# Kernel tuning notes

Measured on AMD Instinct MI355X. Metric: run time of the kernel, lower is better.

## Reference

```python
import jax, jax.numpy as jnp
import numpy as np

M, N, IN, H, NC = 2048, 64, 16, 256, 64
OUT = 3 * NC
NUM_LAYERS = 2


def _lstm_layer(x, Wih, Whh, bih, bhh):
    # x: (M, T, F); Wih: (4H, F); Whh: (4H, H). Torch gate order: i, f, g, o.
    xg = jnp.einsum('mtf,gf->mtg', x, Wih) + bih + bhh  # (M, T, 4H)
    h0 = jnp.zeros((x.shape[0], Whh.shape[1]), x.dtype)

    def step(carry, xt):
        h, c = carry
        gates = xt + h @ Whh.T
        i, f, g, o = jnp.split(gates, 4, axis=-1)
        c = jax.nn.sigmoid(f) * c + jax.nn.sigmoid(i) * jnp.tanh(g)
        h = jax.nn.sigmoid(o) * jnp.tanh(c)
        return (h, c), h

    (_, _), hs = jax.lax.scan(step, (h0, h0), jnp.swapaxes(xg, 0, 1))
    return jnp.swapaxes(hs, 0, 1)  # (M, T, H)


def setup_inputs() -> dict:
    key = jax.random.key(0)
    ks = jax.random.split(key, 12)
    s = 1.0 / np.sqrt(H)
    d = {
        'z': jax.random.normal(ks[0], (M, N, IN), jnp.float32),
        'Wih0': jax.random.normal(ks[1], (4 * H, IN), jnp.float32) * s,
        'Whh0': jax.random.normal(ks[2], (4 * H, H), jnp.float32) * s,
        'bih0': jax.random.normal(ks[3], (4 * H,), jnp.float32) * s,
        'bhh0': jax.random.normal(ks[4], (4 * H,), jnp.float32) * s,
        'Wih1': jax.random.normal(ks[5], (4 * H, H), jnp.float32) * s,
        'Whh1': jax.random.normal(ks[6], (4 * H, H), jnp.float32) * s,
        'bih1': jax.random.normal(ks[7], (4 * H,), jnp.float32) * s,
        'bhh1': jax.random.normal(ks[8], (4 * H,), jnp.float32) * s,
        'fcW': jax.random.normal(ks[9], (OUT, H), jnp.float32) * 0.02,
        'fcb': jax.random.normal(ks[10], (OUT,), jnp.float32) * 0.02,
    }
    return d


def reference(z, Wih0, Whh0, bih0, bhh0, Wih1, Whh1, bih1, bhh1, fcW, fcb):
    h = _lstm_layer(z, Wih0, Whh0, bih0, bhh0)
    h = _lstm_layer(h, Wih1, Whh1, bih1, bhh1)
    y = jnp.einsum('mth,oh->mto', h, fcW) + fcb  # (M, N, 3*NC)

    gammas = jax.nn.softmax(y[..., :NC], axis=2)
    sigmas = jnp.exp(y[..., NC:2 * NC])
    mus = y[..., 2 * NC:]

    key = jax.random.key(42)
    k1, k2 = jax.random.split(key)
    idx = jax.random.categorical(k1, jnp.log(gammas), axis=-1)  # (M, N)
    chosen_mu = jnp.take_along_axis(mus, idx[..., None], axis=2)     # (M, N, 1)
    chosen_sig = jnp.take_along_axis(sigmas, idx[..., None], axis=2)
    eps = jax.random.normal(k2, chosen_mu.shape, jnp.float32)
    x_pred = jax.lax.stop_gradient(chosen_mu + chosen_sig * eps)  # Normal.sample (no grad)

    kern_exp = (x_pred - mus) ** 2                         # broadcast repeat over NC
    kernels = jnp.exp(-0.5 * kern_exp) / sigmas ** 2
    kernels = kernels / ((2.0 * jnp.pi) ** (N / 2) * sigmas ** N)
    x_cond_prob = jnp.einsum('mtc,mtc->mt', gammas, kernels)  # (M, N)
    return x_pred, x_cond_prob
```

## Files before the change

kernel.cpp:

```cpp
#include <hip/hip_runtime.h>
#include <stdint.h>
#include <stddef.h>

#define Mdim 2048
#define Tdim 64
#define INdim 16
#define Hdim 256
#define NCdim 64
#define NUG 64
#define HSLAB (256 * 2048)
#define RSLOTS 16

typedef __attribute__((ext_vector_type(8))) short s16x8;
typedef __attribute__((ext_vector_type(4))) float f32x4;

#define PANEL_US (3 * 16 * 8 * 512)
#define SPOFF 65536
#define BFRAG_US (3 * 8 * 3 * 512)

#define OFF_BFRAG 0
#define OFF_WZ    1179648
#define OFF_BB    (OFF_WZ + 64 * 256)
#define OFF_WFCP  (OFF_BB + 64 * 32)
#define OFF_H0P   (OFF_WFCP + 256 * 64 * 4)
#define OFF_C0    (OFF_H0P + 1572864)
#define OFF_C1    (OFF_C0 + HSLAB)
#define OFF_RINGF (OFF_C1 + HSLAB)
#define OFF_RING2 (OFF_RINGF + 12582912)
#define WS_TOT    (OFF_RING2 + RSLOTS * HSLAB)

#define ROTL32(v, s) (((v) << (s)) | ((v) >> (32 - (s))))

__host__ __device__ inline void tf2x32(uint32_t k0, uint32_t k1, uint32_t x0, uint32_t x1,
                                       uint32_t* o0, uint32_t* o1) {
  uint32_t ks2 = k0 ^ k1 ^ 0x1BD11BDAu;
  x0 += k0; x1 += k1;
  x0 += x1; x1 = ROTL32(x1, 13); x1 ^= x0;
  x0 += x1; x1 = ROTL32(x1, 15); x1 ^= x0;
  x0 += x1; x1 = ROTL32(x1, 26); x1 ^= x0;
  x0 += x1; x1 = ROTL32(x1, 6);  x1 ^= x0;
  x0 += k1; x1 += ks2 + 1u;
  x0 += x1; x1 = ROTL32(x1, 17); x1 ^= x0;
  x0 += x1; x1 = ROTL32(x1, 29); x1 ^= x0;
  x0 += x1; x1 = ROTL32(x1, 16); x1 ^= x0;
  x0 += x1; x1 = ROTL32(x1, 24); x1 ^= x0;
  x0 += ks2; x1 += k0 + 2u;
  x0 += x1; x1 = ROTL32(x1, 13); x1 ^= x0;
  x0 += x1; x1 = ROTL32(x1, 15); x1 ^= x0;
  x0 += x1; x1 = ROTL32(x1, 26); x1 ^= x0;
  x0 += x1; x1 = ROTL32(x1, 6);  x1 ^= x0;
  x0 += k0; x1 += k1 + 3u;
  x0 += x1; x1 = ROTL32(x1, 17); x1 ^= x0;
  x0 += x1; x1 = ROTL32(x1, 29); x1 ^= x0;
  x0 += x1; x1 = ROTL32(x1, 16); x1 ^= x0;
  x0 += x1; x1 = ROTL32(x1, 24); x1 ^= x0;
  x0 += k1; x1 += ks2 + 4u;
  x0 += x1; x1 = ROTL32(x1, 13); x1 ^= x0;
  x0 += x1; x1 = ROTL32(x1, 15); x1 ^= x0;
  x0 += x1; x1 = ROTL32(x1, 26); x1 ^= x0;
  x0 += x1; x1 = ROTL32(x1, 6);  x1 ^= x0;
  x0 += ks2; x1 += k0 + 5u;
  *o0 = x0; *o1 = x1;
}

__device__ inline uint32_t random_bits32(uint32_t ka, uint32_t kb, uint32_t p) {
  uint32_t a, b;
  tf2x32(ka, kb, 0u, p, &a, &b);
  return a ^ b;
}

__device__ inline float bits_to_u01(uint32_t bits) {
  return __uint_as_float((bits >> 9) | 0x3f800000u) - 1.0f;
}

__device__ inline float sigm_fast(float x) { return 1.0f / (1.0f + __expf(-x)); }

__device__ inline float erfinv_f32(float x) {
  float w = -log1pf(-x * x);
  float p;
  if (w < 5.0f) {
    w -= 2.5f;
    p = 2.81022636e-08f;
    p = fmaf(p, w, 3.43273939e-07f);
    p = fmaf(p, w, -3.5233877e-06f);
    p = fmaf(p, w, -4.39150654e-06f);
    p = fmaf(p, w, 0.00021858087f);
    p = fmaf(p, w, -0.00125372503f);
    p = fmaf(p, w, -0.00417768164f);
    p = fmaf(p, w, 0.246640727f);
    p = fmaf(p, w, 1.50140941f);
  } else {
    w = sqrtf(w) - 3.0f;
    p = -0.000200214257f;
    p = fmaf(p, w, 0.000100950558f);
    p = fmaf(p, w, 0.00134934322f);
    p = fmaf(p, w, -0.00367342844f);
    p = fmaf(p, w, 0.00573950773f);
    p = fmaf(p, w, -0.0076224613f);
    p = fmaf(p, w, 0.00943887047f);
    p = fmaf(p, w, 1.00167406f);
    p = fmaf(p, w, 2.83297682f);
  }
  return p * x;
}

__device__ inline void mdn_head(float yg, float ysg, float ym, int lane, uint32_t rid,
                                uint32_t k1a, uint32_t k1b, uint32_t k2a, uint32_t k2b,
                                float* __restrict__ out) {
  uint32_t pp = rid * (uint32_t)NCdim + (uint32_t)lane;
  uint32_t bits = random_bits32(k1a, k1b, pp);
  float u01 = bits_to_u01(bits);
  const float tinyf = 1.17549435e-38f;
  float uu = fmaxf(tinyf, u01 + tinyf);
  float gum = -logf(-logf(uu));
  float val = gum + yg;
  int idx = lane;
#pragma unroll
  for (int s = 1; s < 64; s <<= 1) {
    float ov = __shfl_xor(val, s);
    int oi = __shfl_xor(idx, s);
    if (ov > val || (ov == val && oi < idx)) { val = ov; idx = oi; }
  }
  float mu_sel = __shfl(ym, idx);
  float s_sel = __shfl(ysg, idx);

  uint32_t ebits = random_bits32(k2a, k2b, rid);
  float ue = bits_to_u01(ebits);
  const float lo = __uint_as_float(0xBF7FFFFFu);
  float un2 = fmaxf(lo, ue * 2.0f + lo);
  float eps = 1.41421356f * erfinv_f32(un2);

  float x_pred = mu_sel + expf(s_sel) * eps;

  float mx = yg;
#pragma unroll
  for (int s = 1; s < 64; s <<= 1) mx = fmaxf(mx, __shfl_xor(mx, s));
  float se = expf(yg - mx);
#pragma unroll
  for (int s = 1; s < 64; s <<= 1) se += __shfl_xor(se, s);
  float d = x_pred - ym;
  float lk = -0.5f * d * d - 66.0f * ysg - 58.812066f;
  float ts = expf(yg - mx + lk);
#pragma unroll
  for (int s = 1; s < 64; s <<= 1) ts += __shfl_xor(ts, s);
  float prob = ts / se;

  if (lane == 0) {
    out[rid] = x_pred;
    out[(size_t)Mdim * Tdim + rid] = prob;
  }
}

__device__ __host__ inline unsigned short bf16_trunc(float x) {
  union { float f; uint32_t u; } c; c.f = x;
  return (unsigned short)(c.u >> 16);
}
__device__ __host__ inline float bf16_tof(unsigned short s) {
  union { float f; uint32_t u; } c; c.u = ((uint32_t)s) << 16;
  return c.f;
}

__global__ void vfpg_prep(const float* __restrict__ Wih0, const float* __restrict__ Whh0,
                          const float* __restrict__ Wih1, const float* __restrict__ Whh1,
                          const float* __restrict__ fcW, const float* __restrict__ bih0,
                          const float* __restrict__ bhh0, const float* __restrict__ bih1,
                          const float* __restrict__ bhh1, float* __restrict__ ws) {
  int i0 = blockIdx.x * blockDim.x + threadIdx.x;
  int n = blockDim.x * gridDim.x;
  unsigned short* BF = (unsigned short*)(ws + OFF_BFRAG);
  for (int i = i0; i < 64 * 3 * 8 * 512; i += n) {
    int ug = i / 12288, r = i % 12288;
    int cls = r / 4096, r2 = r % 4096;
    int kt = r2 >> 9, pos = r2 & 511;
    int l = pos >> 3, e = pos & 7;
    int n16 = l & 15, lg = l >> 4;
    int k = kt * 32 + lg * 8 + e;
    int ul = n16 >> 2, ty = n16 & 3;
    int gd = ty * 256 + ug * 4 + ul;
    const float* W = (cls == 0) ? Whh0 : ((cls == 1) ? Wih1 : Whh1);
    float w = W[gd * 256 + k];
    unsigned short s0 = bf16_trunc(w);
    float r1 = w - bf16_tof(s0);
    unsigned short s1 = bf16_trunc(r1);
    unsigned short s2 = bf16_trunc(r1 - bf16_tof(s1));
    size_t base = ((size_t)(ug * 3 + cls) * 8 + kt) * (3 * 512) + pos;
    BF[base] = s0;
    BF[base + 512] = s1;
    BF[base + 1024] = s2;
  }
  for (int i = i0; i < 64 * 256; i += n) {
    int ug = i >> 8, k = (i >> 4) & 15, g = i & 15;
    int gd = (g & 3) * 256 + ug * 4 + (g >> 2);
    ws[OFF_WZ + i] = Wih0[gd * INdim + k];
  }
  for (int i = i0; i < 64 * 32; i += n) {
    int ug = i >> 5, r = i & 31, g = r & 15;
    int gd = (g & 3) * 256 + ug * 4 + (g >> 2);
    ws[OFF_BB + i] = (r < 16) ? (bih0[gd] + bhh0[gd]) : (bih1[gd] + bhh1[gd]);
  }
  float4* wfcp = (float4*)(ws + OFF_WFCP);
  for (int o = i0; o < 256 * 64; o += n) {
    int k = o >> 6, c = o & 63;
    wfcp[o] = make_float4(fcW[c * Hdim + k], fcW[(64 + c) * Hdim + k],
                          fcW[(128 + c) * Hdim + k], 0.0f);
  }
}

__device__ inline void cell1s(float gi, float gf, float gg, float go, float cold,
                              float* cn, float* hn) {
  float si = sigm_fast(gi), sf = sigm_fast(gf);
  float tg = fmaf(2.0f, sigm_fast(2.0f * gg), -1.0f);
  float so = sigm_fast(go);
  float cc = fmaf(sf, cold, si * tg);
  *cn = cc;
  *hn = so * fmaf(2.0f, sigm_fast(2.0f * cc), -1.0f);
}

#define GBS2 33

template <int MODE>
__launch_bounds__(512, 2)
__global__ void vfpg_step(const float* __restrict__ z, const float* __restrict__ ws,
                          float* __restrict__ wsm, int t) {
  __shared__ unsigned short lB01[2 * 2 * 8 * 2 * 512];
  __shared__ __align__(16) unsigned char uni[81920];
  __shared__ float lz[2 * 256];
  __shared__ float lbias[64];

  const int tid = threadIdx.x;
  const int rg = blockIdx.x & 7, ugc = blockIdx.x >> 3;
  const int mb = rg * 256;
  const int lane = tid & 63, wid = tid >> 6;
  float* gbuf = (float*)uni;

  {
    const unsigned short* BF = (const unsigned short*)(ws + OFF_BFRAG);
    const unsigned short* BG0 = BF + (size_t)(ugc * 2 + 0) * BFRAG_US;
    const unsigned short* BG1 = BF + (size_t)(ugc * 2 + 1) * BFRAG_US;
    for (int i = tid; i < 2 * 4608; i += 512) {
      int ugl = i / 4608;
      int r = i % 4608;
      int cls = r / 1536;
      int r2 = r % 1536;
      int kt = r2 / 192;
      int sp = (r2 / 64) % 3;
      int v = r2 & 63;
      const unsigned short* src = (ugl ? BG1 : BG0) + ((size_t)(cls * 8 + kt) * 3 + sp) * 512 + v * 8;
      s16x8 val = *(const s16x8*)src;
      if (cls < 2 && sp < 2) {
        ((s16x8*)lB01)[((((ugl * 2 + cls) * 8 + kt) * 2 + sp)) * 64 + v] = val;
      } else {
        int str = (cls == 2) ? (2 + sp) : cls;
        ((s16x8*)uni)[(((ugl * 5 + str) * 8 + kt)) * 64 + v] = val;
      }
    }
    if (tid < 128) ((float4*)lz)[tid] = ((const float4*)(ws + OFF_WZ + (ugc * 2) * 256))[tid];
    if (tid < 64) lbias[tid] = ws[OFF_BB + (ugc * 2) * 32 + tid];
  }
  __syncthreads();

  f32x4 aL0[2][2], aL1[2][2];
#pragma unroll
  for (int i = 0; i < 2; i++)
#pragma unroll
    for (int u = 0; u < 2; u++) { aL0[i][u] = (f32x4)0.0f; aL1[i][u] = (f32x4)0.0f; }

  if (MODE >= 1) {
    const unsigned short* p0 = (const unsigned short*)(ws + OFF_H0P) +
                               ((size_t)((t - 1) & 1) * 8 + rg) * PANEL_US;
    const unsigned short* p1 = (const unsigned short*)(ws + OFF_RINGF) +
                               ((size_t)((t - 2) & 15) * 8 + rg) * PANEL_US;
    const bool doH1 = (t >= 2);
    const s16x8* pL = (const s16x8*)lB01;
    const s16x8* pU = (const s16x8*)uni;

    s16x8 Ab0[6], Ab1[6];
    {
      size_t fb = ((size_t)(wid * 2) * 8 + 0) * 512 + lane * 8;
      Ab0[0] = *(const s16x8*)(p0 + fb);
      Ab0[1] = *(const s16x8*)(p0 + fb + SPOFF);
      Ab0[2] = *(const s16x8*)(p0 + fb + 2 * SPOFF);
      if (doH1) {
        Ab0[3] = *(const s16x8*)(p1 + fb);
        Ab0[4] = *(const s16x8*)(p1 + fb + SPOFF);
        Ab0[5] = *(const s16x8*)(p1 + fb + 2 * SPOFF);
      }
    }

#pragma unroll 1
    for (int kt = 0; kt < 8; kt++) {
      s16x8 bL0s0[2], bL0s1[2], bL0s2[2], bIs0[2], bIs1[2], bIs2[2], bHs0[2], bHs1[2], bHs2[2];
#pragma unroll
      for (int u = 0; u < 2; u++) {
        if (MODE == 1) {
          bL0s0[u] = pL[(((u * 2 + 0) * 8 + kt) * 2 + 0) * 64 + lane];
          bL0s1[u] = pL[(((u * 2 + 0) * 8 + kt) * 2 + 1) * 64 + lane];
          bL0s2[u] = pU[((u * 5 + 0) * 8 + kt) * 64 + lane];
        }
        bIs0[u] = pL[(((u * 2 + 1) * 8 + kt) * 2 + 0) * 64 + lane];
        bIs1[u] = pL[(((u * 2 + 1) * 8 + kt) * 2 + 1) * 64 + lane];
        bIs2[u] = pU[((u * 5 + 1) * 8 + kt) * 64 + lane];
        if (doH1) {
          bHs0[u] = pU[((u * 5 + 2) * 8 + kt) * 64 + lane];
          bHs1[u] = pU[((u * 5 + 3) * 8 + kt) * 64 + lane];
          bHs2[u] = pU[((u * 5 + 4) * 8 + kt) * 64 + lane];
        }
      }
#pragma unroll
      for (int i = 0; i < 2; i++) {
        s16x8* cur = (i & 1) ? Ab1 : Ab0;
        s16x8* nxt = (i & 1) ? Ab0 : Ab1;
        int nkt = (i < 1) ? kt : kt + 1;
        int ni = (i < 1) ? 1 : 0;
        if (nkt < 8) {
          size_t fb = ((size_t)(wid * 2 + ni) * 8 + nkt) * 512 + lane * 8;
          nxt[0] = *(const s16x8*)(p0 + fb);
          nxt[1] = *(const s16x8*)(p0 + fb + SPOFF);
          nxt[2] = *(const s16x8*)(p0 + fb + 2 * SPOFF);
          if (doH1) {
            nxt[3] = *(const s16x8*)(p1 + fb);
            nxt[4] = *(const s16x8*)(p1 + fb + SPOFF);
            nxt[5] = *(const s16x8*)(p1 + fb + 2 * SPOFF);
          }
        }
        s16x8 a0 = cur[0], a1 = cur[1], a2 = cur[2];
#pragma unroll
        for (int u = 0; u < 2; u++) {
          if (MODE == 1) {
            aL0[i][u] = __builtin_amdgcn_mfma_f32_16x16x32_bf16(a0, bL0s0[u], aL0[i][u], 0, 0, 0);
            aL0[i][u] = __builtin_amdgcn_mfma_f32_16x16x32_bf16(a0, bL0s1[u], aL0[i][u], 0, 0, 0);
            aL0[i][u] = __builtin_amdgcn_mfma_f32_16x16x32_bf16(a1, bL0s0[u], aL0[i][u], 0, 0, 0);
            aL0[i][u] = __builtin_amdgcn_mfma_f32_16x16x32_bf16(a1, bL0s1[u], aL0[i][u], 0, 0, 0);
            aL0[i][u] = __builtin_amdgcn_mfma_f32_16x16x32_bf16(a0, bL0s2[u], aL0[i][u], 0, 0, 0);
            aL0[i][u] = __builtin_amdgcn_mfma_f32_16x16x32_bf16(a2, bL0s0[u], aL0[i][u], 0, 0, 0);
          }
          aL1[i][u] = __builtin_amdgcn_mfma_f32_16x16x32_bf16(a0, bIs0[u], aL1[i][u], 0, 0, 0);
          aL1[i][u] = __builtin_amdgcn_mfma_f32_16x16x32_bf16(a0, bIs1[u], aL1[i][u], 0, 0, 0);
          aL1[i][u] = __builtin_amdgcn_mfma_f32_16x16x32_bf16(a1, bIs0[u], aL1[i][u], 0, 0, 0);
          aL1[i][u] = __builtin_amdgcn_mfma_f32_16x16x32_bf16(a1, bIs1[u], aL1[i][u], 0, 0, 0);
          aL1[i][u] = __builtin_amdgcn_mfma_f32_16x16x32_bf16(a0, bIs2[u], aL1[i][u], 0, 0, 0);
          aL1[i][u] = __builtin_amdgcn_mfma_f32_16x16x32_bf16(a2, bIs0[u], aL1[i][u], 0, 0, 0);
          if (doH1) {
            s16x8 c0 = cur[3], c1 = cur[4], c2 = cur[5];
            aL1[i][u] = __builtin_amdgcn_mfma_f32_16x16x32_bf16(c0, bHs0[u], aL1[i][u], 0, 0, 0);
            aL1[i][u] = __builtin_amdgcn_mfma_f32_16x16x32_bf16(c0, bHs1[u], aL1[i][u], 0, 0, 0);
            aL1[i][u] = __builtin_amdgcn_mfma_f32_16x16x32_bf16(c1, bHs0[u], aL1[i][u], 0, 0, 0);
            aL1[i][u] = __builtin_amdgcn_mfma_f32_16x16x32_bf16(c1, bHs1[u], aL1[i][u], 0, 0, 0);
            aL1[i][u] = __builtin_amdgcn_mfma_f32_16x16x32_bf16(c0, bHs2[u], aL1[i][u], 0, 0, 0);
            aL1[i][u] = __builtin_amdgcn_mfma_f32_16x16x32_bf16(c2, bHs0[u], aL1[i][u], 0, 0, 0);
          }
        }
      }
    }
  }
  __syncthreads();

  float* c0w = wsm + OFF_C0;
  float* c1w = wsm + OFF_C1;
  const int ugl = tid >> 8;
  const int mloc = tid & 255;
  const int m = mb + mloc;
  const int ug = ugc * 2 + ugl;
  const int mtc = mloc >> 4, mrowc = mloc & 15;
  const int ktw = ug >> 3;
  const int lgw = (ug & 7) >> 1;
  const int ebase = (ug * 4) & 7;
  const int lww = lgw * 16 + mrowc;
  const size_t fo = ((size_t)mtc * 8 + ktw) * 512 + lww * 8 + ebase;

  if (MODE <= 1) {
    if (MODE == 1) {
      int col = lane & 15, rb2 = (lane >> 4) * 4;
#pragma unroll
      for (int i = 0; i < 2; i++)
#pragma unroll
        for (int u = 0; u < 2; u++)
#pragma unroll
          for (int j = 0; j < 4; j++)
            gbuf[((wid * 2 + i) * 16 + rb2 + j) * GBS2 + u * 16 + col] = aL0[i][u][j];
    }
    __syncthreads();
    float zr[16];
#pragma unroll
    for (int f4 = 0; f4 < 4; f4++)
      *(float4*)&zr[f4 * 4] = *(const float4*)&z[(size_t)m * 1024 + t * 16 + f4 * 4];
    float g16[16];
#pragma unroll
    for (int gg = 0; gg < 16; gg++)
      g16[gg] = lbias[ugl * 32 + gg] + ((MODE == 1) ? gbuf[mloc * GBS2 + ugl * 16 + gg] : 0.0f);
    const float* lzu = lz + ugl * 256;
#pragma unroll
    for (int f = 0; f < 16; f++) {
      float zv = zr[f];
      float4 w0 = *(const float4*)&lzu[f * 16 + 0];
      float4 w1 = *(const float4*)&lzu[f * 16 + 4];
      float4 w2 = *(const float4*)&lzu[f * 16 + 8];
      float4 w3 = *(const float4*)&lzu[f * 16 + 12];
      g16[0] = fmaf(zv, w0.x, g16[0]);  g16[1] = fmaf(zv, w0.y, g16[1]);
      g16[2] = fmaf(zv, w0.z, g16[2]);  g16[3] = fmaf(zv, w0.w, g16[3]);
      g16[4] = fmaf(zv, w1.x, g16[4]);  g16[5] = fmaf(zv, w1.y, g16[5]);
      g16[6] = fmaf(zv, w1.z, g16[6]);  g16[7] = fmaf(zv, w1.w, g16[7]);
      g16[8] = fmaf(zv, w2.x, g16[8]);  g16[9] = fmaf(zv, w2.y, g16[9]);
      g16[10] = fmaf(zv, w2.z, g16[10]); g16[11] = fmaf(zv, w2.w, g16[11]);
      g16[12] = fmaf(zv, w3.x, g16[12]); g16[13] = fmaf(zv, w3.y, g16[13]);
      g16[14] = fmaf(zv, w3.z, g16[14]); g16[15] = fmaf(zv, w3.w, g16[15]);
    }
    unsigned short* wp = (unsigned short*)(wsm + OFF_H0P) +
                         ((size_t)(t & 1) * 8 + rg) * PANEL_US;
    short sp0[4], sp1[4], sp2[4];
#pragma unroll
    for (int ul = 0; ul < 4; ul++) {
      int u = ug * 4 + ul;
      size_t cidx = (size_t)u * 2048 + m;
      float cold = (MODE == 1) ? c0w[cidx] : 0.0f;
      float cn, hn;
      cell1s(g16[ul * 4 + 0], g16[ul * 4 + 1], g16[ul * 4 + 2], g16[ul * 4 + 3], cold, &cn, &hn);
      c0w[cidx] = cn;
      unsigned short s0 = bf16_trunc(hn);
      float r1 = hn - bf16_tof(s0);
      unsigned short s1 = bf16_trunc(r1);
      unsigned short s2 = bf16_trunc(r1 - bf16_tof(s1));
      sp0[ul] = (short)s0; sp1[ul] = (short)s1; sp2[ul] = (short)s2;
    }
    *(short4*)&wp[fo]             = make_short4(sp0[0], sp0[1], sp0[2], sp0[3]);
    *(short4*)&wp[fo + SPOFF]     = make_short4(sp1[0], sp1[1], sp1[2], sp1[3]);
    *(short4*)&wp[fo + 2 * SPOFF] = make_short4(sp2[0], sp2[1], sp2[2], sp2[3]);
    __syncthreads();
  }

  if (MODE >= 1) {
    {
      int col = lane & 15, rb2 = (lane >> 4) * 4;
#pragma unroll
      for (int i = 0; i < 2; i++)
#pragma unroll
        for (int u = 0; u < 2; u++)
#pragma unroll
          for (int j = 0; j < 4; j++)
            gbuf[((wid * 2 + i) * 16 + rb2 + j) * GBS2 + u * 16 + col] = aL1[i][u][j];
    }
    __syncthreads();
    int slot = (t - 1) & 15;
    unsigned short* rp = (unsigned short*)(wsm + OFF_RINGF) +
                         ((size_t)slot * 8 + rg) * PANEL_US;
    float* r2 = wsm + OFF_RING2 + (size_t)slot * HSLAB;
    float h4[4];
    short sp0[4], sp1[4], sp2[4];
#pragma unroll
    for (int ul = 0; ul < 4; ul++) {
      float gi = lbias[ugl * 32 + 16 + ul * 4 + 0] + gbuf[mloc * GBS2 + ugl * 16 + ul * 4 + 0];
      float gf = lbias[ugl * 32 + 16 + ul * 4 + 1] + gbuf[mloc * GBS2 + ugl * 16 + ul * 4 + 1];
      float gt = lbias[ugl * 32 + 16 + ul * 4 + 2] + gbuf[mloc * GBS2 + ugl * 16 + ul * 4 + 2];
      float go = lbias[ugl * 32 + 16 + ul * 4 + 3] + gbuf[mloc * GBS2 + ugl * 16 + ul * 4 + 3];
      int u = ug * 4 + ul;
      size_t cidx = (size_t)u * 2048 + m;
      float cold = (t >= 2) ? c1w[cidx] : 0.0f;
      float cn, hn;
      cell1s(gi, gf, gt, go, cold, &cn, &hn);
      c1w[cidx] = cn;
      h4[ul] = hn;
      unsigned short s0 = bf16_trunc(hn);
      float r1v = hn - bf16_tof(s0);
      unsigned short s1 = bf16_trunc(r1v);
      unsigned short s2 = bf16_trunc(r1v - bf16_tof(s1));
      sp0[ul] = (short)s0; sp1[ul] = (short)s1; sp2[ul] = (short)s2;
    }
    *(short4*)&rp[fo]             = make_short4(sp0[0], sp0[1], sp0[2], sp0[3]);
    *(short4*)&rp[fo + SPOFF]     = make_short4(sp1[0], sp1[1], sp1[2], sp1[3]);
    *(short4*)&rp[fo + 2 * SPOFF] = make_short4(sp2[0], sp2[1], sp2[2], sp2[3]);
    *(float4*)&r2[(size_t)m * 256 + ug * 4] = make_float4(h4[0], h4[1], h4[2], h4[3]);
  }
}

__launch_bounds__(512, 2)
__global__ void vfpg_head(const float* __restrict__ ws, const float* __restrict__ fcb,
                          float* __restrict__ out, int tbase,
                          uint32_t k1a, uint32_t k1b, uint32_t k2a, uint32_t k2b) {
  __shared__ __align__(16) float hsw[8][8][Hdim];
  const int tid = threadIdx.x;
  const int lane = tid & 63, wid = tid >> 6;
  const int rb8 = blockIdx.x * 8 + wid;
  const int slot = rb8 >> 8;
  const int mbase = (rb8 & 255) * 8;

  const float* r2 = ws + OFF_RING2 + (size_t)slot * HSLAB + (size_t)mbase * 256;
  const float4* WFCP = (const float4*)(ws + OFF_WFCP);

#pragma unroll
  for (int rr = 0; rr < 8; rr++)
    *(float4*)&hsw[wid][rr][lane * 4] = *(const float4*)&r2[rr * 256 + lane * 4];
  __builtin_amdgcn_s_waitcnt(0);

  float yg[8], ys[8], ym[8];
#pragma unroll
  for (int rr = 0; rr < 8; rr++) {
    yg[rr] = fcb[lane]; ys[rr] = fcb[64 + lane]; ym[rr] = fcb[128 + lane];
  }
#pragma unroll 2
  for (int k4 = 0; k4 < 64; k4++) {
    float4 h4[8];
#pragma unroll
    for (int rr = 0; rr < 8; rr++) h4[rr] = *(const float4*)&hsw[wid][rr][k4 * 4];
#pragma unroll
    for (int j = 0; j < 4; j++) {
      float4 w = WFCP[(k4 * 4 + j) * 64 + lane];
#pragma unroll
      for (int rr = 0; rr < 8; rr++) {
        float hv = (&h4[rr].x)[j];
        yg[rr] = fmaf(hv, w.x, yg[rr]);
        ys[rr] = fmaf(hv, w.y, ys[rr]);
        ym[rr] = fmaf(hv, w.z, ym[rr]);
      }
    }
  }
  int tt = tbase + slot;
#pragma unroll 1
  for (int rr = 0; rr < 8; rr++) {
    uint32_t rid = (uint32_t)(mbase + rr) * Tdim + (uint32_t)tt;
    mdn_head(yg[rr], ys[rr], ym[rr], lane, rid, k1a, k1b, k2a, k2b, out);
  }
}

extern "C" void kernel_launch(void* const* d_in, const int* in_sizes, int n_in,
                              void* d_out, int out_size, void* d_ws, size_t ws_size,
                              hipStream_t stream) {
  const float* z    = (const float*)d_in[0];
  const float* Wih0 = (const float*)d_in[1];
  const float* Whh0 = (const float*)d_in[2];
  const float* bih0 = (const float*)d_in[3];
  const float* bhh0 = (const float*)d_in[4];
  const float* Wih1 = (const float*)d_in[5];
  const float* Whh1 = (const float*)d_in[6];
  const float* bih1 = (const float*)d_in[7];
  const float* bhh1 = (const float*)d_in[8];
  const float* fcW  = (const float*)d_in[9];
  const float* fcb  = (const float*)d_in[10];
  float* ws = (float*)d_ws;
  float* out = (float*)d_out;

  if (ws_size < (size_t)WS_TOT * sizeof(float)) return;

  vfpg_prep<<<dim3(512), dim3(256), 0, stream>>>(
      Wih0, Whh0, Wih1, Whh1, fcW, bih0, bhh0, bih1, bhh1, ws);

  uint32_t k1a, k1b, k2a, k2b;
  tf2x32(0u, 42u, 0u, 0u, &k1a, &k1b);
  tf2x32(0u, 42u, 0u, 1u, &k2a, &k2b);

  vfpg_step<0><<<dim3(256), dim3(512), 0, stream>>>(z, ws, ws, 0);
  for (int t = 1; t <= 63; t++) {
    vfpg_step<1><<<dim3(256), dim3(512), 0, stream>>>(z, ws, ws, t);
    if (t == 16 || t == 32 || t == 48) {
      vfpg_head<<<dim3(512), dim3(512), 0, stream>>>(ws, fcb, out, t - 16,
                                                     k1a, k1b, k2a, k2b);
    }
  }
  vfpg_step<2><<<dim3(256), dim3(512), 0, stream>>>(z, ws, ws, 64);
  vfpg_head<<<dim3(512), dim3(512), 0, stream>>>(ws, fcb, out, 48, k1a, k1b, k2a, k2b);
}
```

Measured before the change: 2.069 ms.

## Compute FC head with split-bf16 MFMA from the hidden-state ring, separate sampling kernel

```diff
diff --git a/kernel.cpp b/kernel.cpp
--- a/kernel.cpp
+++ b/kernel.cpp
@@ -26,8 +26,9 @@
 #define OFF_C0    (OFF_H0P + 1572864)
 #define OFF_C1    (OFF_C0 + HSLAB)
 #define OFF_RINGF (OFF_C1 + HSLAB)
-#define OFF_RING2 (OFF_RINGF + 12582912)
-#define WS_TOT    (OFF_RING2 + RSLOTS * HSLAB)
+#define OFF_Y     (OFF_RINGF + 12582912)
+#define OFF_FCB3  (OFF_Y + RSLOTS * HSLAB)
+#define WS_TOT    (OFF_FCB3 + 73728)
 
 #define ROTL32(v, s) (((v) << (s)) | ((v) >> (32 - (s))))
 
@@ -198,11 +199,22 @@
     int gd = (g & 3) * 256 + ug * 4 + (g >> 2);
     ws[OFF_BB + i] = (r < 16) ? (bih0[gd] + bhh0[gd]) : (bih1[gd] + bhh1[gd]);
   }
-  float4* wfcp = (float4*)(ws + OFF_WFCP);
-  for (int o = i0; o < 256 * 64; o += n) {
-    int k = o >> 6, c = o & 63;
-    wfcp[o] = make_float4(fcW[c * Hdim + k], fcW[(64 + c) * Hdim + k],
-                          fcW[(128 + c) * Hdim + k], 0.0f);
+  unsigned short* BFC = (unsigned short*)(ws + OFF_FCB3);
+  for (int i = i0; i < 12 * 8 * 512; i += n) {
+    int ntkt = i >> 9, pos = i & 511;
+    int nt = ntkt >> 3, kt = ntkt & 7;
+    int l = pos >> 3, e = pos & 7;
+    int c = nt * 16 + (l & 15);
+    int k = kt * 32 + (l >> 4) * 8 + e;
+    float w = fcW[c * Hdim + k];
+    unsigned short s0 = bf16_trunc(w);
+    float r1 = w - bf16_tof(s0);
+    unsigned short s1 = bf16_trunc(r1);
+    unsigned short s2 = bf16_trunc(r1 - bf16_tof(s1));
+    size_t base = (size_t)ntkt * (3 * 512) + pos;
+    BFC[base] = s0;
+    BFC[base + 512] = s1;
+    BFC[base + 1024] = s2;
   }
 }
 
@@ -443,8 +455,6 @@
     int slot = (t - 1) & 15;
     unsigned short* rp = (unsigned short*)(wsm + OFF_RINGF) +
                          ((size_t)slot * 8 + rg) * PANEL_US;
-    float* r2 = wsm + OFF_RING2 + (size_t)slot * HSLAB;
-    float h4[4];
     short sp0[4], sp1[4], sp2[4];
 #pragma unroll
     for (int ul = 0; ul < 4; ul++) {
@@ -458,7 +468,6 @@
       float cn, hn;
       cell1s(gi, gf, gt, go, cold, &cn, &hn);
       c1w[cidx] = cn;
-      h4[ul] = hn;
       unsigned short s0 = bf16_trunc(hn);
       float r1v = hn - bf16_tof(s0);
       unsigned short s1 = bf16_trunc(r1v);
@@ -468,57 +477,80 @@
     *(short4*)&rp[fo]             = make_short4(sp0[0], sp0[1], sp0[2], sp0[3]);
     *(short4*)&rp[fo + SPOFF]     = make_short4(sp1[0], sp1[1], sp1[2], sp1[3]);
     *(short4*)&rp[fo + 2 * SPOFF] = make_short4(sp2[0], sp2[1], sp2[2], sp2[3]);
-    *(float4*)&r2[(size_t)m * 256 + ug * 4] = make_float4(h4[0], h4[1], h4[2], h4[3]);
   }
 }
 
 __launch_bounds__(512, 2)
-__global__ void vfpg_head(const float* __restrict__ ws, const float* __restrict__ fcb,
+__global__ void vfpg_fc(const float* __restrict__ ws, float* __restrict__ wsm) {
+  const int tid = threadIdx.x;
+  const int rg = blockIdx.x & 7;
+  const int slot = (blockIdx.x >> 3) & 15;
+  const int mtg = blockIdx.x >> 7;
+  const int lane = tid & 63, wid = tid >> 6;
+  const int mt = mtg * 8 + wid;
+
+  const unsigned short* pa = (const unsigned short*)(ws + OFF_RINGF) +
+                             ((size_t)slot * 8 + rg) * PANEL_US;
+  const unsigned short* BFC = (const unsigned short*)(ws + OFF_FCB3);
+  float* y = wsm + OFF_Y + (size_t)slot * (2048 * 192) + (size_t)(rg * 256) * 192;
+
+  const int col = lane & 15, rb2 = (lane >> 4) * 4;
+
+#pragma unroll 1
+  for (int ng = 0; ng < 3; ng++) {
+    f32x4 C[4];
+#pragma unroll
+    for (int j = 0; j < 4; j++) C[j] = (f32x4)0.0f;
+#pragma unroll 1
+    for (int kt = 0; kt < 8; kt++) {
+      size_t fb = ((size_t)mt * 8 + kt) * 512 + lane * 8;
+      s16x8 a0 = *(const s16x8*)(pa + fb);
+      s16x8 a1 = *(const s16x8*)(pa + fb + SPOFF);
+      s16x8 a2 = *(const s16x8*)(pa + fb + 2 * SPOFF);
+#pragma unroll
+      for (int n4 = 0; n4 < 4; n4++) {
+        int nt = ng * 4 + n4;
+        const unsigned short* bp = BFC + (size_t)(nt * 8 + kt) * (3 * 512) + lane * 8;
+        s16x8 b0 = *(const s16x8*)(bp);
+        s16x8 b1 = *(const s16x8*)(bp + 512);
+        s16x8 b2 = *(const s16x8*)(bp + 1024);
+        C[n4] = __builtin_amdgcn_mfma_f32_16x16x32_bf16(a0, b0, C[n4], 0, 0, 0);
+        C[n4] = __builtin_amdgcn_mfma_f32_16x16x32_bf16(a0, b1, C[n4], 0, 0, 0);
+        C[n4] = __builtin_amdgcn_mfma_f32_16x16x32_bf16(a1, b0, C[n4], 0, 0, 0);
+        C[n4] = __builtin_amdgcn_mfma_f32_16x16x32_bf16(a1, b1, C[n4], 0, 0, 0);
+        C[n4] = __builtin_amdgcn_mfma_f32_16x16x32_bf16(a0, b2, C[n4], 0, 0, 0);
+        C[n4] = __builtin_amdgcn_mfma_f32_16x16x32_bf16(a2, b0, C[n4], 0, 0, 0);
+      }
+    }
+#pragma unroll
+    for (int n4 = 0; n4 < 4; n4++) {
+      int c = (ng * 4 + n4) * 16 + col;
+#pragma unroll
+      for (int j = 0; j < 4; j++) {
+        int mrow = mt * 16 + rb2 + j;
+        y[(size_t)mrow * 192 + c] = C[n4][j];
+      }
+    }
+  }
+}
+
+__launch_bounds__(512, 2)
+__global__ void vfpg_samp(const float* __restrict__ ws, const float* __restrict__ fcb,
                           float* __restrict__ out, int tbase,
                           uint32_t k1a, uint32_t k1b, uint32_t k2a, uint32_t k2b) {
-  __shared__ __align__(16) float hsw[8][8][Hdim];
   const int tid = threadIdx.x;
   const int lane = tid & 63, wid = tid >> 6;
-  const int rb8 = blockIdx.x * 8 + wid;
-  const int slot = rb8 >> 8;
-  const int mbase = (rb8 & 255) * 8;
-
-  const float* r2 = ws + OFF_RING2 + (size_t)slot * HSLAB + (size_t)mbase * 256;
-  const float4* WFCP = (const float4*)(ws + OFF_WFCP);
-
-#pragma unroll
-  for (int rr = 0; rr < 8; rr++)
-    *(float4*)&hsw[wid][rr][lane * 4] = *(const float4*)&r2[rr * 256 + lane * 4];
-  __builtin_amdgcn_s_waitcnt(0);
-
-  float yg[8], ys[8], ym[8];
-#pragma unroll
-  for (int rr = 0; rr < 8; rr++) {
-    yg[rr] = fcb[lane]; ys[rr] = fcb[64 + lane]; ym[rr] = fcb[128 + lane];
-  }
-#pragma unroll 2
-  for (int k4 = 0; k4 < 64; k4++) {
-    float4 h4[8];
-#pragma unroll
-    for (int rr = 0; rr < 8; rr++) h4[rr] = *(const float4*)&hsw[wid][rr][k4 * 4];
-#pragma unroll
-    for (int j = 0; j < 4; j++) {
-      float4 w = WFCP[(k4 * 4 + j) * 64 + lane];
-#pragma unroll
-      for (int rr = 0; rr < 8; rr++) {
-        float hv = (&h4[rr].x)[j];
-        yg[rr] = fmaf(hv, w.x, yg[rr]);
-        ys[rr] = fmaf(hv, w.y, ys[rr]);
-        ym[rr] = fmaf(hv, w.z, ym[rr]);
-      }
-    }
-  }
-  int tt = tbase + slot;
-#pragma unroll 1
-  for (int rr = 0; rr < 8; rr++) {
-    uint32_t rid = (uint32_t)(mbase + rr) * Tdim + (uint32_t)tt;
-    mdn_head(yg[rr], ys[rr], ym[rr], lane, rid, k1a, k1b, k2a, k2b, out);
-  }
+  const int ridx = blockIdx.x * 8 + wid;
+  const int slot = ridx >> 11;
+  const int m = ridx & 2047;
+
+  const float* yrow = ws + OFF_Y + (size_t)ridx * 192;
+  float yg = yrow[lane] + fcb[lane];
+  float ys = yrow[64 + lane] + fcb[64 + lane];
+  float ym = yrow[128 + lane] + fcb[128 + lane];
+
+  uint32_t rid = (uint32_t)m * Tdim + (uint32_t)(tbase + slot);
+  mdn_head(yg, ys, ym, lane, rid, k1a, k1b, k2a, k2b, out);
 }
 
 extern "C" void kernel_launch(void* const* d_in, const int* in_sizes, int n_in,
@@ -551,10 +583,12 @@
   for (int t = 1; t <= 63; t++) {
     vfpg_step<1><<<dim3(256), dim3(512), 0, stream>>>(z, ws, ws, t);
     if (t == 16 || t == 32 || t == 48) {
-      vfpg_head<<<dim3(512), dim3(512), 0, stream>>>(ws, fcb, out, t - 16,
-                                                     k1a, k1b, k2a, k2b);
+      vfpg_fc<<<dim3(256), dim3(512), 0, stream>>>(ws, ws);
+      vfpg_samp<<<dim3(4096), dim3(512), 0, stream>>>(ws, fcb, out, t - 16,
+                                                      k1a, k1b, k2a, k2b);
     }
   }
   vfpg_step<2><<<dim3(256), dim3(512), 0, stream>>>(z, ws, ws, 64);
-  vfpg_head<<<dim3(512), dim3(512), 0, stream>>>(ws, fcb, out, 48, k1a, k1b, k2a, k2b);
-}
+  vfpg_fc<<<dim3(256), dim3(512), 0, stream>>>(ws, ws);
+  vfpg_samp<<<dim3(4096), dim3(512), 0, stream>>>(ws, fcb, out, 48, k1a, k1b, k2a, k2b);
+}
```

Result: faster. 1.932 ms (-6.6%).
